# Optimization experiments

Measured on AMD Instinct MI355X. Metric: run time of the kernel, lower is better.

The kernel has to match this reference:

```python
import jax, jax.numpy as jnp
import numpy as np

N, NN, NI, ND, NH = 20000, 32, 128, 128, 8
RADIUS = 1.0
EPS = 1e-5


def _mlp(x, W1, b1, W2, b2):
    return jax.nn.elu(x @ W1 + b1) @ W2 + b2


def setup_inputs() -> dict:
    key = jax.random.key(0)
    ks = jax.random.split(key, 32)
    s = 0.05
    inp = {
        "features": jax.random.normal(ks[0], (N, NI), jnp.float32),
        "x": jax.random.normal(ks[1], (N, 3), jnp.float32),
        "nuv": jax.random.normal(ks[2], (N, 3, 3), jnp.float32),
        "topk": jax.random.randint(ks[3], (N, NN), 0, N, jnp.int64),
        # query_f: Ni -> Nd -> Nh*Nd
        "qW1": jax.random.normal(ks[4], (NI, ND), jnp.float32) * s,
        "qb1": jnp.zeros((ND,), jnp.float32),
        "qW2": jax.random.normal(ks[5], (ND, NH * ND), jnp.float32) * s,
        "qb2": jnp.zeros((NH * ND,), jnp.float32),
        # geo_encoder: 12 -> Nd -> Nd
        "gW1": jax.random.normal(ks[6], (12, ND), jnp.float32) * s,
        "gb1": jnp.zeros((ND,), jnp.float32),
        "gW2": jax.random.normal(ks[7], (ND, ND), jnp.float32) * s,
        "gb2": jnp.zeros((ND,), jnp.float32),
        # key_f / value_f: Nd -> Nd -> Nd
        "kW1": jax.random.normal(ks[8], (ND, ND), jnp.float32) * s,
        "kb1": jnp.zeros((ND,), jnp.float32),
        "kW2": jax.random.normal(ks[9], (ND, ND), jnp.float32) * s,
        "kb2": jnp.zeros((ND,), jnp.float32),
        "vW1": jax.random.normal(ks[10], (ND, ND), jnp.float32) * s,
        "vb1": jnp.zeros((ND,), jnp.float32),
        "vW2": jax.random.normal(ks[11], (ND, ND), jnp.float32) * s,
        "vb2": jnp.zeros((ND,), jnp.float32),
        # decode_f: Nh*Nd -> Nd -> Nd
        "dW1": jax.random.normal(ks[12], (NH * ND, ND), jnp.float32) * s,
        "db1": jnp.zeros((ND,), jnp.float32),
        "dW2": jax.random.normal(ks[13], (ND, ND), jnp.float32) * s,
        "db2": jnp.zeros((ND,), jnp.float32),
        # LayerNorm
        "ln_g": jnp.ones((ND,), jnp.float32),
        "ln_b": jnp.zeros((ND,), jnp.float32),
    }
    return inp


def reference(features, x, nuv, topk, qW1, qb1, qW2, qb2, gW1, gb1, gW2, gb2,
              kW1, kb1, kW2, kb2, vW1, vb1, vW2, vb2, dW1, db1, dW2, db2,
              ln_g, ln_b):
    n, nn = topk.shape
    sdk = jnp.sqrt(jnp.float32(ND))

    Q = _mlp(features, qW1, qb1, qW2, qb2).reshape(n, NH, ND)  # (N,Nh,Nd)

    features_nn = features[topk]              # (N,nn,Nd)
    x_nn = x[topk]                            # (N,nn,3)
    orient_x = x_nn - x[:, None, :]           # (N,nn,3)
    nuv_nn = nuv[topk].reshape(n, nn * 3, 3)  # (N,nn*3,3)

    dis2 = jnp.sum(orient_x * orient_x, axis=2, keepdims=True)
    dis = jnp.exp(-dis2 / (2.0 * RADIUS * RADIUS))  # (N,nn,1)

    # rotate neighbor offsets / frames into local frame: nuv @ v^T, then transpose
    RL_x = jnp.einsum('nij,nkj->nki', nuv, orient_x)            # (N,nn,3)
    RL_nuv = jnp.einsum('nij,nkj->nki', nuv, nuv_nn)            # (N,nn*3,3)
    RL_nuv = RL_nuv.reshape(n, nn, 9)
    RL = jnp.concatenate([RL_x, RL_nuv], axis=-1)               # (N,nn,12)

    geo_fea = _mlp(RL, gW1, gb1, gW2, gb2)
    geo_fea = dis * geo_fea * features_nn                       # (N,nn,Nd)

    K = _mlp(geo_fea, kW1, kb1, kW2, kb2)                       # (N,nn,Nd)
    V = _mlp(geo_fea, vW1, vb1, vW2, vb2)                       # (N,nn,Nd)

    Mq = jnp.einsum('nhd,nkd->nhk', Q, K)                       # (N,Nh,nn)
    mask = (topk == 0)[:, None, :]                              # (N,1,nn)
    Mq = jnp.where(mask, -jnp.inf, Mq)
    Mq = jax.nn.softmax(Mq / sdk, axis=2)

    out = jnp.einsum('nhk,nkd->nhd', Mq, V).reshape(n, NH * ND)
    out = _mlp(out, dW1, db1, dW2, db2) + features

    mu = jnp.mean(out, axis=-1, keepdims=True)
    var = jnp.var(out, axis=-1, keepdims=True)
    return (out - mu) / jnp.sqrt(var + EPS) * ln_g + ln_b
```

## Files before the change

kernel.cpp:

```cpp
#include <hip/hip_runtime.h>
#include <math.h>
#include <stdint.h>

#define ND 128
#define NNB 32
#define NH 8

typedef __attribute__((ext_vector_type(8))) short bf16x8;
typedef __attribute__((ext_vector_type(4))) float f32x4;
typedef __attribute__((ext_vector_type(8))) unsigned short u16x8;
typedef unsigned short u16;
typedef unsigned int u32;
typedef unsigned long long u64;

#define OFF_QW1T 0ULL
#define OFF_QW2T 32768ULL
#define OFF_GW1T 294912ULL
#define OFF_GW2T 303104ULL
#define OFF_KW1T 335872ULL
#define OFF_KW2T 368640ULL
#define OFF_VW1T 401408ULL
#define OFF_VW2T 434176ULL
#define OFF_DW1T 466944ULL
#define OFF_DW2T 729088ULL
#define OFF_Q    761856ULL
#define OFF_ATT  (OFF_Q + 20096ULL * 2048ULL)

__device__ __forceinline__ u16 rneb(float f){
    u32 u = __builtin_bit_cast(u32, f);
    u32 r = u + 0x7fffu + ((u >> 16) & 1u);
    return (u16)(r >> 16);
}
__device__ __forceinline__ float elu_f(float v){ return v > 0.f ? v : (__expf(v) - 1.f); }
__device__ __forceinline__ u64 pack4(float a, float b, float c, float d){
    return (u64)rneb(a) | ((u64)rneb(b) << 16) | ((u64)rneb(c) << 32) | ((u64)rneb(d) << 48);
}

#define GLDS16(g, l) __builtin_amdgcn_global_load_lds( \
    (const __attribute__((address_space(1))) u32*)(g), \
    (__attribute__((address_space(3))) u32*)(u32)(u64)(l), 16, 0, 0)

__device__ __forceinline__ void stage_rows(char* lds, const char* g, size_t gstride){
    const int t = threadIdx.x;
    const int seg = (t & 15) * 16, rr = t >> 4;
    #pragma unroll
    for (int i = 0; i < 8; i++){
        int row = i * 16 + rr;
        GLDS16(g + (size_t)row * gstride + seg, lds + row * 256 + seg);
    }
}

__device__ __forceinline__ bf16x8 ldfrag(const u16* base, int row, int kb, int l){
    int r = row + (l & 15);
    int byte = (r << 8) + (((kb << 1) + ((l >> 4) << 4)) ^ ((r & 7) << 4));
    return *(const bf16x8*)((const char*)base + byte);
}
__device__ __forceinline__ bf16x8 ldfragG(const char* __restrict__ Wt, int n, int kstride, int kb, int l){
    return *(const bf16x8*)(Wt + (size_t)(n + (l & 15)) * (size_t)kstride
                               + (size_t)((kb << 1) + ((l >> 4) << 4)));
}
__device__ __forceinline__ bf16x8 ldfragRL(const u16* base, int row, int l){
    int r = row + (l & 15);
    int byte = (r << 6) + ((((l >> 4) << 4)) ^ ((r & 3) << 4));
    return *(const bf16x8*)((const char*)base + byte);
}

__device__ __forceinline__ void store_cfrag(u16* out, int m0t, int n0t, int l, f32x4 v){
    int col = n0t + (l & 15);
    int r0 = m0t + ((l >> 4) << 2);
    #pragma unroll
    for (int j = 0; j < 4; j++){
        int r = r0 + j;
        int byte = (r << 8) + (((col << 1)) ^ ((r & 7) << 4));
        *(u16*)((char*)out + byte) = rneb(v[j]);
    }
}
__device__ __forceinline__ void store_cfragT(u16* out, int m0t, int n0t, int l, f32x4 v){
    int c = n0t + (l & 15);
    int r0 = m0t + ((l >> 4) << 2);
    *(u64*)((char*)out + (c << 8) + (((r0 << 1)) ^ ((c & 7) << 4))) = pack4(v[0], v[1], v[2], v[3]);
}

__device__ __forceinline__ void gemm_tileG(const u16* A, const char* __restrict__ Wt,
                                           int kstride, int kbase, f32x4 acc[4][4]){
    const int t = threadIdx.x, l = t & 63;
    const int m0 = ((t >> 7) & 1) * 64;
    const int n0 = ((t >> 6) & 1) * 64;
    bf16x8 b[4][4];
    #pragma unroll
    for (int kk = 0; kk < 4; kk++)
        #pragma unroll
        for (int i = 0; i < 4; i++)
            b[kk][i] = ldfragG(Wt, n0 + i * 16, kstride, kbase + kk * 32, l);
    #pragma unroll
    for (int kk = 0; kk < 4; kk++){
        bf16x8 a[4];
        #pragma unroll
        for (int i = 0; i < 4; i++) a[i] = ldfrag(A, m0 + i * 16, kk * 32, l);
        #pragma unroll
        for (int mt = 0; mt < 4; mt++)
            #pragma unroll
            for (int nt = 0; nt < 4; nt++)
                acc[mt][nt] = __builtin_amdgcn_mfma_f32_16x16x32_bf16(a[mt], b[kk][nt], acc[mt][nt], 0, 0, 0);
    }
}

struct PrepDesc {
    const float* src[10];
    u64 dstoff[10];
    int N[10], Ksrc[10], Kdst[10];
};

__global__ __launch_bounds__(256) void prep_weights(PrepDesc d, char* ws){
    int tid = blockIdx.x * 256 + threadIdx.x;
    #pragma unroll 1
    for (int m = 0; m < 10; m++){
        int cnt = (d.Kdst[m] * d.N[m]) >> 3;
        if (tid < cnt){
            int N = d.N[m];
            int nn = tid % N, k8 = tid / N;
            const float* s = d.src[m];
            u16x8 pk;
            #pragma unroll
            for (int i = 0; i < 8; i++){
                int k = k8 * 8 + i;
                pk[i] = (k < d.Ksrc[m]) ? rneb(s[(size_t)k * N + nn]) : (u16)0;
            }
            *(u16x8*)(ws + d.dstoff[m] + (u64)nn * (u64)(d.Kdst[m] * 2) + (u64)(k8 * 16)) = pk;
            return;
        }
        tid -= cnt;
    }
}

__global__ __launch_bounds__(256, 2) void qmlp_kernel(
    const float* __restrict__ F, const float* __restrict__ qb1, const float* __restrict__ qb2,
    const char* __restrict__ ws, u16* __restrict__ Qg, int n)
{
    __shared__ __align__(16) u16 sIn[16384];
    __shared__ __align__(16) u16 sH[16384];
    const int t = threadIdx.x;
    const int row0 = blockIdx.x * 128;
    const int l = t & 63;
    const int m0 = ((t >> 7) & 1) * 64;
    const int n0 = ((t >> 6) & 1) * 64;

    for (int i = t; i < 4096; i += 256){
        int r = i >> 5, c = (i & 31) * 4;
        int gr = row0 + r;
        float4 v = make_float4(0.f, 0.f, 0.f, 0.f);
        if (gr < n) v = *(const float4*)&F[(size_t)gr * ND + c];
        *(u64*)((char*)sIn + (r << 8) + (((c << 1)) ^ ((r & 7) << 4))) = pack4(v.x, v.y, v.z, v.w);
    }
    __syncthreads();

    f32x4 acc[4][4];
    #pragma unroll
    for (int i = 0; i < 4; i++)
        #pragma unroll
        for (int j = 0; j < 4; j++) acc[i][j] = 0.f;
    gemm_tileG(sIn, ws + OFF_QW1T, 256, 0, acc);
    #pragma unroll
    for (int mt = 0; mt < 4; mt++)
        #pragma unroll
        for (int nt = 0; nt < 4; nt++){
            int col = n0 + nt * 16 + (l & 15);
            float bv = qb1[col];
            f32x4 v;
            #pragma unroll
            for (int j = 0; j < 4; j++) v[j] = elu_f(acc[mt][nt][j] + bv);
            store_cfrag(sH, m0 + mt * 16, n0 + nt * 16, l, v);
        }
    __syncthreads();

    for (int ct = 0; ct < 8; ct++){
        f32x4 a2[4][4];
        #pragma unroll
        for (int i = 0; i < 4; i++)
            #pragma unroll
            for (int j = 0; j < 4; j++) a2[i][j] = 0.f;
        gemm_tileG(sH, ws + OFF_QW2T + (u64)ct * 32768ULL, 256, 0, a2);
        #pragma unroll
        for (int mt = 0; mt < 4; mt++)
            #pragma unroll
            for (int nt = 0; nt < 4; nt++){
                int col = n0 + nt * 16 + (l & 15);
                float bv = qb2[ct * 128 + col];
                int r0 = m0 + mt * 16 + ((l >> 4) << 2);
                #pragma unroll
                for (int j = 0; j < 4; j++)
                    *(u16*)((char*)sIn + ((r0 + j) << 8) + (col << 1)) = rneb(a2[mt][nt][j] + bv);
            }
        __syncthreads();
        {
            int row = t >> 1, half = t & 1;
            int gr = row0 + row;
            if (gr < n){
                const char* src = (const char*)sIn + (row << 8) + half * 128;
                char* dst = (char*)Qg + (size_t)gr * 2048 + ct * 256 + half * 128;
                #pragma unroll
                for (int i = 0; i < 8; i++)
                    *(uint4*)(dst + i * 16) = *(const uint4*)(src + i * 16);
            }
        }
        __syncthreads();
    }
}

template<int ACT>
__device__ __forceinline__ void layerG(
    const u16* inB, u16* outB, const char* __restrict__ Wt,
    const float* __restrict__ bias, const float* __restrict__ F,
    const int* sidx, const float* sdis)
{
    const int t = threadIdx.x, l = t & 63;
    const int m0 = ((t >> 7) & 1) * 64;
    const int n0 = ((t >> 6) & 1) * 64;
    f32x4 acc[4][4];
    #pragma unroll
    for (int i = 0; i < 4; i++)
        #pragma unroll
        for (int j = 0; j < 4; j++) acc[i][j] = 0.f;
    gemm_tileG(inB, Wt, 256, 0, acc);
    float fv[4][4][4];
    if (ACT == 2){
        #pragma unroll
        for (int mt = 0; mt < 4; mt++)
            #pragma unroll
            for (int nt = 0; nt < 4; nt++){
                int col = n0 + nt * 16 + (l & 15);
                int r0 = m0 + mt * 16 + ((l >> 4) << 2);
                #pragma unroll
                for (int j = 0; j < 4; j++){
                    int r = r0 + j;
                    fv[mt][nt][j] = sdis[r] * F[(size_t)sidx[r] * ND + col];
                }
            }
    }
    __syncthreads();
    #pragma unroll
    for (int mt = 0; mt < 4; mt++)
        #pragma unroll
        for (int nt = 0; nt < 4; nt++){
            int col = n0 + nt * 16 + (l & 15);
            float bv = bias[col];
            f32x4 v;
            #pragma unroll
            for (int j = 0; j < 4; j++){
                float x = acc[mt][nt][j] + bv;
                if (ACT == 1) x = elu_f(x);
                if (ACT == 2) x = x * fv[mt][nt][j];
                v[j] = x;
            }
            if (ACT == 3) store_cfragT(outB, m0 + mt * 16, n0 + nt * 16, l, v);
            else          store_cfrag (outB, m0 + mt * 16, n0 + nt * 16, l, v);
        }
    __syncthreads();
}

__global__ __launch_bounds__(256, 2) void attn_kernel(
    const float* __restrict__ F, const float* __restrict__ X,
    const float* __restrict__ NUV, const int* __restrict__ TOPK,
    const float* __restrict__ gb1, const float* __restrict__ gb2,
    const float* __restrict__ kb1, const float* __restrict__ kb2,
    const float* __restrict__ vb1, const float* __restrict__ vb2,
    const char* __restrict__ ws, const u16* __restrict__ Qg, u16* __restrict__ ATT)
{
    __shared__ __align__(16) u16 buf0[16384];
    __shared__ __align__(16) u16 buf1[16384];
    __shared__ __align__(16) u16 sP16[2560];
    __shared__ float sdis[128];
    __shared__ int   sidx[128];

    const int t = threadIdx.x;
    const int pid0 = blockIdx.x * 4;

    if (t < 128){
        int p = t >> 5, k = t & 31;
        int pid = pid0 + p;
        int idx = TOPK[(size_t)pid * NNB + k];
        sidx[t] = idx;
        float x0 = X[(size_t)pid * 3 + 0], x1 = X[(size_t)pid * 3 + 1], x2 = X[(size_t)pid * 3 + 2];
        float ox = X[(size_t)idx * 3 + 0] - x0;
        float oy = X[(size_t)idx * 3 + 1] - x1;
        float oz = X[(size_t)idx * 3 + 2] - x2;
        sdis[t] = __expf(-0.5f * (ox * ox + oy * oy + oz * oz));
        float nv[9];
        #pragma unroll
        for (int i = 0; i < 9; i++) nv[i] = NUV[(size_t)pid * 9 + i];
        float f[12];
        #pragma unroll
        for (int i = 0; i < 3; i++)
            f[i] = nv[i * 3 + 0] * ox + nv[i * 3 + 1] * oy + nv[i * 3 + 2] * oz;
        #pragma unroll
        for (int r = 0; r < 3; r++){
            float a0 = NUV[(size_t)idx * 9 + r * 3 + 0];
            float a1 = NUV[(size_t)idx * 9 + r * 3 + 1];
            float a2 = NUV[(size_t)idx * 9 + r * 3 + 2];
            #pragma unroll
            for (int i = 0; i < 3; i++)
                f[3 + r * 3 + i] = nv[i * 3 + 0] * a0 + nv[i * 3 + 1] * a1 + nv[i * 3 + 2] * a2;
        }
        char* rb = (char*)buf1 + (t << 6);
        u32 key = (u32)(t & 3) << 4;
        *(u64*)(rb + (0u ^ key))  = pack4(f[0], f[1], f[2], f[3]);
        *(u64*)(rb + (8u ^ key))  = pack4(f[4], f[5], f[6], f[7]);
        *(u64*)(rb + (16u ^ key)) = pack4(f[8], f[9], f[10], f[11]);
        *(u64*)(rb + (24u ^ key)) = 0ULL;
        *(u64*)(rb + (32u ^ key)) = 0ULL;
        *(u64*)(rb + (40u ^ key)) = 0ULL;
        *(u64*)(rb + (48u ^ key)) = 0ULL;
        *(u64*)(rb + (56u ^ key)) = 0ULL;
    }
    __syncthreads();

    {
        const int l = t & 63;
        const int m0 = ((t >> 7) & 1) * 64;
        const int n0 = ((t >> 6) & 1) * 64;
        bf16x8 bg[4], ag[4];
        #pragma unroll
        for (int i = 0; i < 4; i++) bg[i] = ldfragG(ws + OFF_GW1T, n0 + i * 16, 64, 0, l);
        #pragma unroll
        for (int i = 0; i < 4; i++) ag[i] = ldfragRL(buf1, m0 + i * 16, l);
        f32x4 acc[4][4];
        #pragma unroll
        for (int i = 0; i < 4; i++)
            #pragma unroll
            for (int j = 0; j < 4; j++) acc[i][j] = 0.f;
        #pragma unroll
        for (int mt = 0; mt < 4; mt++)
            #pragma unroll
            for (int nt = 0; nt < 4; nt++)
                acc[mt][nt] = __builtin_amdgcn_mfma_f32_16x16x32_bf16(ag[mt], bg[nt], acc[mt][nt], 0, 0, 0);
        #pragma unroll
        for (int mt = 0; mt < 4; mt++)
            #pragma unroll
            for (int nt = 0; nt < 4; nt++){
                int col = n0 + nt * 16 + (l & 15);
                float bv = gb1[col];
                f32x4 v;
                #pragma unroll
                for (int j = 0; j < 4; j++) v[j] = elu_f(acc[mt][nt][j] + bv);
                store_cfrag(buf0, m0 + mt * 16, n0 + nt * 16, l, v);
            }
    }
    __syncthreads();

    layerG<2>(buf0, buf0, ws + OFF_GW2T, gb2, F, sidx, sdis);
    layerG<1>(buf0, buf1, ws + OFF_KW1T, kb1, F, sidx, sdis);
    layerG<0>(buf1, buf1, ws + OFF_KW2T, kb2, F, sidx, sdis);
    layerG<1>(buf0, buf0, ws + OFF_VW1T, vb1, F, sidx, sdis);
    layerG<3>(buf0, buf0, ws + OFF_VW2T, vb2, F, sidx, sdis);

    {
        const int l = t & 63, w = t >> 6, hi = l >> 4;
        f32x4 s0, s1;
        s0 = 0.f; s1 = 0.f;
        const char* qb = (const char*)Qg + (size_t)(pid0 + w) * 2048
                       + (size_t)(l & 7) * 256 + (size_t)(hi << 4);
        #pragma unroll
        for (int kk = 0; kk < 4; kk++){
            bf16x8 bq = *(const bf16x8*)(qb + kk * 64);
            bf16x8 a0 = ldfrag(buf1, w * 32,      kk * 32, l);
            bf16x8 a1 = ldfrag(buf1, w * 32 + 16, kk * 32, l);
            s0 = __builtin_amdgcn_mfma_f32_16x16x32_bf16(a0, bq, s0, 0, 0, 0);
            s1 = __builtin_amdgcn_mfma_f32_16x16x32_bf16(a1, bq, s1, 0, 0, 0);
        }
        const float RS = 0.08838834764831845f;
        float sv[8];
        #pragma unroll
        for (int mt = 0; mt < 2; mt++)
            #pragma unroll
            for (int j = 0; j < 4; j++){
                int kidx = mt * 16 + (hi << 2) + j;
                float x = (mt ? s1[j] : s0[j]) * RS;
                if (sidx[w * 32 + kidx] == 0) x = -INFINITY;
                sv[mt * 4 + j] = x;
            }
        float mx = sv[0];
        #pragma unroll
        for (int i = 1; i < 8; i++) mx = fmaxf(mx, sv[i]);
        mx = fmaxf(mx, __shfl_xor(mx, 16));
        mx = fmaxf(mx, __shfl_xor(mx, 32));
        float e[8], sum = 0.f;
        #pragma unroll
        for (int i = 0; i < 8; i++){ e[i] = __expf(sv[i] - mx); sum += e[i]; }
        sum += __shfl_xor(sum, 16);
        sum += __shfl_xor(sum, 32);
        float inv = 1.f / sum;
        int h = l & 15;
        char* pb = (char*)sP16 + w * 1280 + h * 80 + hi * 8;
        *(u64*)(pb)      = pack4(e[0] * inv, e[1] * inv, e[2] * inv, e[3] * inv);
        *(u64*)(pb + 32) = pack4(e[4] * inv, e[5] * inv, e[6] * inv, e[7] * inv);
    }
    __syncthreads();

    {
        const int l = t & 63, w = t >> 6, hi = l >> 4;
        bf16x8 pa = *(const bf16x8*)((const char*)sP16 + w * 1280 + (l & 15) * 80 + (hi << 4));
        int pid = pid0 + w;
        u32 key = ((u32)pid & 7) << 4;
        char* dst = (char*)ATT + (size_t)pid * 2048;
        #pragma unroll
        for (int nt = 0; nt < 8; nt++){
            f32x4 o;
            o = 0.f;
            bf16x8 bv = ldfrag(buf0, nt * 16, w * 32, l);
            o = __builtin_amdgcn_mfma_f32_16x16x32_bf16(pa, bv, o, 0, 0, 0);
            if (hi < 2){
                int d = nt * 16 + (l & 15);
                #pragma unroll
                for (int j = 0; j < 4; j++){
                    int h = hi * 4 + j;
                    *(u16*)(dst + h * 256 + (((u32)(d << 1)) ^ key)) = rneb(o[j]);
                }
            }
        }
    }
}

__global__ __launch_bounds__(256, 2) void decode_kernel(
    const u16* __restrict__ ATT,
    const float* __restrict__ db1, const float* __restrict__ db2,
    const float* __restrict__ F,
    const float* __restrict__ lng, const float* __restrict__ lnb,
    const char* __restrict__ ws, float* __restrict__ OUT, int n)
{
    __shared__ __align__(16) char SM[67584];
    u16* sA = (u16*)SM;
    u16* sH = (u16*)(SM + 32768);
    float* sO = (float*)SM;

    const int t = threadIdx.x;
    const int row0 = blockIdx.x * 128;
    const int l = t & 63;
    const int m0 = ((t >> 7) & 1) * 64;
    const int n0 = ((t >> 6) & 1) * 64;

    f32x4 acc[4][4];
    #pragma unroll
    for (int i = 0; i < 4; i++)
        #pragma unroll
        for (int j = 0; j < 4; j++) acc[i][j] = 0.f;
    for (int kc = 0; kc < 8; kc++){
        stage_rows((char*)sA, (const char*)ATT + (size_t)row0 * 2048 + kc * 256, 2048);
        __syncthreads();
        gemm_tileG(sA, ws + OFF_DW1T, 2048, kc * 128, acc);
        __syncthreads();
    }
    #pragma unroll
    for (int mt = 0; mt < 4; mt++)
        #pragma unroll
        for (int nt = 0; nt < 4; nt++){
            int col = n0 + nt * 16 + (l & 15);
            float bv = db1[col];
            f32x4 v;
            #pragma unroll
            for (int j = 0; j < 4; j++) v[j] = elu_f(acc[mt][nt][j] + bv);
            store_cfrag(sH, m0 + mt * 16, n0 + nt * 16, l, v);
        }
    __syncthreads();

    f32x4 a2[4][4];
    #pragma unroll
    for (int i = 0; i < 4; i++)
        #pragma unroll
        for (int j = 0; j < 4; j++) a2[i][j] = 0.f;
    gemm_tileG(sH, ws + OFF_DW2T, 256, 0, a2);
    __syncthreads();

    #pragma unroll
    for (int mt = 0; mt < 4; mt++)
        #pragma unroll
        for (int nt = 0; nt < 4; nt++){
            int col = n0 + nt * 16 + (l & 15);
            float bv = db2[col];
            int r0 = m0 + mt * 16 + ((l >> 4) << 2);
            #pragma unroll
            for (int j = 0; j < 4; j++){
                int r = r0 + j;
                int gr = row0 + r;
                float x = a2[mt][nt][j] + bv;
                if (gr < n) x += F[(size_t)gr * ND + col];
                sO[r * 132 + col] = x;
            }
        }
    __syncthreads();

    {
        int r = t >> 1, half = t & 1;
        const float* rowp = sO + r * 132 + half * 64;
        float s = 0.f;
        #pragma unroll
        for (int i = 0; i < 16; i++){
            float4 v = ((const float4*)rowp)[i];
            s += v.x + v.y + v.z + v.w;
        }
        s += __shfl_xor(s, 1);
        float mu = s * (1.0f / 128.0f);
        float q = 0.f;
        #pragma unroll
        for (int i = 0; i < 16; i++){
            float4 v = ((const float4*)rowp)[i];
            q += (v.x - mu) * (v.x - mu) + (v.y - mu) * (v.y - mu)
               + (v.z - mu) * (v.z - mu) + (v.w - mu) * (v.w - mu);
        }
        q += __shfl_xor(q, 1);
        float rstd = rsqrtf(q * (1.0f / 128.0f) + 1e-5f);
        int gr = row0 + r;
        if (gr < n){
            #pragma unroll
            for (int i = 0; i < 16; i++){
                float4 v = ((const float4*)rowp)[i];
                int c = half * 64 + i * 4;
                float4 g4 = *(const float4*)&lng[c];
                float4 b4 = *(const float4*)&lnb[c];
                float4 ov = make_float4((v.x - mu) * rstd * g4.x + b4.x,
                                        (v.y - mu) * rstd * g4.y + b4.y,
                                        (v.z - mu) * rstd * g4.z + b4.z,
                                        (v.w - mu) * rstd * g4.w + b4.w);
                *(float4*)&OUT[(size_t)gr * ND + c] = ov;
            }
        }
    }
}

extern "C" void kernel_launch(void* const* d_in, const int* in_sizes, int n_in,
                              void* d_out, int out_size, void* d_ws, size_t ws_size,
                              hipStream_t stream)
{
    const float* F    = (const float*)d_in[0];
    const float* X    = (const float*)d_in[1];
    const float* NUV  = (const float*)d_in[2];
    const int*   TOPK = (const int*)d_in[3];
    const float* qW1  = (const float*)d_in[4];
    const float* qb1  = (const float*)d_in[5];
    const float* qW2  = (const float*)d_in[6];
    const float* qb2  = (const float*)d_in[7];
    const float* gW1  = (const float*)d_in[8];
    const float* gb1  = (const float*)d_in[9];
    const float* gW2  = (const float*)d_in[10];
    const float* gb2  = (const float*)d_in[11];
    const float* kW1  = (const float*)d_in[12];
    const float* kb1  = (const float*)d_in[13];
    const float* kW2  = (const float*)d_in[14];
    const float* kb2  = (const float*)d_in[15];
    const float* vW1  = (const float*)d_in[16];
    const float* vb1  = (const float*)d_in[17];
    const float* vW2  = (const float*)d_in[18];
    const float* vb2  = (const float*)d_in[19];
    const float* dW1  = (const float*)d_in[20];
    const float* db1  = (const float*)d_in[21];
    const float* dW2  = (const float*)d_in[22];
    const float* db2  = (const float*)d_in[23];
    const float* lng  = (const float*)d_in[24];
    const float* lnb  = (const float*)d_in[25];

    const int n = in_sizes[0] / ND;
    char* wsb = (char*)d_ws;

    PrepDesc pd;
    const float* srcs[10] = {qW1, qW2, gW1, gW2, kW1, kW2, vW1, vW2, dW1, dW2};
    u64 offs[10] = {OFF_QW1T, OFF_QW2T, OFF_GW1T, OFF_GW2T, OFF_KW1T,
                    OFF_KW2T, OFF_VW1T, OFF_VW2T, OFF_DW1T, OFF_DW2T};
    int Ns[10]   = {128, 1024, 128, 128, 128, 128, 128, 128, 128, 128};
    int Ksrc[10] = {128, 128, 12, 128, 128, 128, 128, 128, 1024, 128};
    int Kdst[10] = {128, 128, 32, 128, 128, 128, 128, 128, 1024, 128};
    for (int i = 0; i < 10; i++){
        pd.src[i] = srcs[i]; pd.dstoff[i] = offs[i];
        pd.N[i] = Ns[i]; pd.Ksrc[i] = Ksrc[i]; pd.Kdst[i] = Kdst[i];
    }
    prep_weights<<<186, 256, 0, stream>>>(pd, wsb);

    u16* Qg  = (u16*)(wsb + OFF_Q);
    u16* ATT = (u16*)(wsb + OFF_ATT);
    const int nb = (n + 127) / 128;

    qmlp_kernel<<<nb, 256, 0, stream>>>(F, qb1, qb2, wsb, Qg, n);
    attn_kernel<<<n / 4, 256, 0, stream>>>(F, X, NUV, TOPK, gb1, gb2,
                                           kb1, kb2, vb1, vb2, wsb, Qg, ATT);
    decode_kernel<<<nb, 256, 0, stream>>>(ATT, db1, db2, F, lng, lnb, wsb, (float*)d_out, n);
}
```

Measured before the change: 410.5 us.

## Swap GEMM operand roles so epilogues write packed transposed outputs

Adds a gemm_WA form in which the weight fragment is the MFMA A operand and the activation is B. Each lane then holds four consecutive output channels of one row, so bias loads become float4, stores become packed 64-bit writes, and gathers of F become vector loads. The attention kernel is reordered: the V MLP now runs after the softmax, using a separate buffer instead of in-place passes, which removes some barriers. s_setprio is wrapped around the MFMA loops. This adds layout complexity and risks LDS bank conflicts on the new store pattern.

```diff
diff --git a/kernel.cpp b/kernel.cpp
--- a/kernel.cpp
+++ b/kernel.cpp
@@ -65,33 +65,44 @@
     return *(const bf16x8*)((const char*)base + byte);
 }
 
-__device__ __forceinline__ void store_cfrag(u16* out, int m0t, int n0t, int l, f32x4 v){
-    int col = n0t + (l & 15);
-    int r0 = m0t + ((l >> 4) << 2);
-    #pragma unroll
-    for (int j = 0; j < 4; j++){
-        int r = r0 + j;
-        int byte = (r << 8) + (((col << 1)) ^ ((r & 7) << 4));
-        *(u16*)((char*)out + byte) = rneb(v[j]);
-    }
-}
-__device__ __forceinline__ void store_cfragT(u16* out, int m0t, int n0t, int l, f32x4 v){
-    int c = n0t + (l & 15);
-    int r0 = m0t + ((l >> 4) << 2);
-    *(u64*)((char*)out + (c << 8) + (((r0 << 1)) ^ ((c & 7) << 4))) = pack4(v[0], v[1], v[2], v[3]);
-}
-
-__device__ __forceinline__ void gemm_tileG(const u16* A, const char* __restrict__ Wt,
-                                           int kstride, int kbase, f32x4 acc[4][4]){
+__device__ __forceinline__ void gemm_WA(const char* __restrict__ Wt, int kstride, int kbase,
+                                        const u16* B, f32x4 acc[4][4]){
     const int t = threadIdx.x, l = t & 63;
     const int m0 = ((t >> 7) & 1) * 64;
     const int n0 = ((t >> 6) & 1) * 64;
-    bf16x8 b[4][4];
+    bf16x8 aw[4][4];
     #pragma unroll
     for (int kk = 0; kk < 4; kk++)
         #pragma unroll
         for (int i = 0; i < 4; i++)
-            b[kk][i] = ldfragG(Wt, n0 + i * 16, kstride, kbase + kk * 32, l);
+            aw[kk][i] = ldfragG(Wt, m0 + i * 16, kstride, kbase + kk * 32, l);
+    __builtin_amdgcn_s_setprio(1);
+    #pragma unroll
+    for (int kk = 0; kk < 4; kk++){
+        bf16x8 b[4];
+        #pragma unroll
+        for (int i = 0; i < 4; i++) b[i] = ldfrag(B, n0 + i * 16, kk * 32, l);
+        #pragma unroll
+        for (int mt = 0; mt < 4; mt++)
+            #pragma unroll
+            for (int nt = 0; nt < 4; nt++)
+                acc[mt][nt] = __builtin_amdgcn_mfma_f32_16x16x32_bf16(aw[kk][mt], b[nt], acc[mt][nt], 0, 0, 0);
+    }
+    __builtin_amdgcn_s_setprio(0);
+}
+
+__device__ __forceinline__ void gemm_AW(const u16* A, const char* __restrict__ Wt,
+                                        f32x4 acc[4][4]){
+    const int t = threadIdx.x, l = t & 63;
+    const int m0 = ((t >> 7) & 1) * 64;
+    const int n0 = ((t >> 6) & 1) * 64;
+    bf16x8 bw[4][4];
+    #pragma unroll
+    for (int kk = 0; kk < 4; kk++)
+        #pragma unroll
+        for (int i = 0; i < 4; i++)
+            bw[kk][i] = ldfragG(Wt, n0 + i * 16, 256, kk * 32, l);
+    __builtin_amdgcn_s_setprio(1);
     #pragma unroll
     for (int kk = 0; kk < 4; kk++){
         bf16x8 a[4];
@@ -101,8 +112,9 @@
         for (int mt = 0; mt < 4; mt++)
             #pragma unroll
             for (int nt = 0; nt < 4; nt++)
-                acc[mt][nt] = __builtin_amdgcn_mfma_f32_16x16x32_bf16(a[mt], b[kk][nt], acc[mt][nt], 0, 0, 0);
-    }
+                acc[mt][nt] = __builtin_amdgcn_mfma_f32_16x16x32_bf16(a[mt], bw[kk][nt], acc[mt][nt], 0, 0, 0);
+    }
+    __builtin_amdgcn_s_setprio(0);
 }
 
 struct PrepDesc {
@@ -144,6 +156,7 @@
     const int l = t & 63;
     const int m0 = ((t >> 7) & 1) * 64;
     const int n0 = ((t >> 6) & 1) * 64;
+    const int hi = l >> 4;
 
     for (int i = t; i < 4096; i += 256){
         int r = i >> 5, c = (i & 31) * 4;
@@ -159,18 +172,19 @@
     for (int i = 0; i < 4; i++)
         #pragma unroll
         for (int j = 0; j < 4; j++) acc[i][j] = 0.f;
-    gemm_tileG(sIn, ws + OFF_QW1T, 256, 0, acc);
-    #pragma unroll
-    for (int mt = 0; mt < 4; mt++)
+    gemm_WA(ws + OFF_QW1T, 256, 0, sIn, acc);
+    #pragma unroll
+    for (int mt = 0; mt < 4; mt++){
+        int ch0 = m0 + mt * 16 + (hi << 2);
+        float4 bq = *(const float4*)&qb1[ch0];
         #pragma unroll
         for (int nt = 0; nt < 4; nt++){
-            int col = n0 + nt * 16 + (l & 15);
-            float bv = qb1[col];
-            f32x4 v;
-            #pragma unroll
-            for (int j = 0; j < 4; j++) v[j] = elu_f(acc[mt][nt][j] + bv);
-            store_cfrag(sH, m0 + mt * 16, n0 + nt * 16, l, v);
-        }
+            int xrow = n0 + nt * 16 + (l & 15);
+            u64 pk = pack4(elu_f(acc[mt][nt][0] + bq.x), elu_f(acc[mt][nt][1] + bq.y),
+                           elu_f(acc[mt][nt][2] + bq.z), elu_f(acc[mt][nt][3] + bq.w));
+            *(u64*)((char*)sH + (xrow << 8) + (((ch0 << 1)) ^ ((xrow & 7) << 4))) = pk;
+        }
+    }
     __syncthreads();
 
     for (int ct = 0; ct < 8; ct++){
@@ -179,18 +193,19 @@
         for (int i = 0; i < 4; i++)
             #pragma unroll
             for (int j = 0; j < 4; j++) a2[i][j] = 0.f;
-        gemm_tileG(sH, ws + OFF_QW2T + (u64)ct * 32768ULL, 256, 0, a2);
-        #pragma unroll
-        for (int mt = 0; mt < 4; mt++)
+        gemm_WA(ws + OFF_QW2T + (u64)ct * 32768ULL, 256, 0, sH, a2);
+        #pragma unroll
+        for (int mt = 0; mt < 4; mt++){
+            int ch0 = m0 + mt * 16 + (hi << 2);
+            float4 bq = *(const float4*)&qb2[ct * 128 + ch0];
             #pragma unroll
             for (int nt = 0; nt < 4; nt++){
-                int col = n0 + nt * 16 + (l & 15);
-                float bv = qb2[ct * 128 + col];
-                int r0 = m0 + mt * 16 + ((l >> 4) << 2);
-                #pragma unroll
-                for (int j = 0; j < 4; j++)
-                    *(u16*)((char*)sIn + ((r0 + j) << 8) + (col << 1)) = rneb(a2[mt][nt][j] + bv);
-            }
+                int xrow = n0 + nt * 16 + (l & 15);
+                *(u64*)((char*)sIn + (xrow << 8) + (ch0 << 1)) =
+                    pack4(a2[mt][nt][0] + bq.x, a2[mt][nt][1] + bq.y,
+                          a2[mt][nt][2] + bq.z, a2[mt][nt][3] + bq.w);
+            }
+        }
         __syncthreads();
         {
             int row = t >> 1, half = t & 1;
@@ -207,8 +222,8 @@
     }
 }
 
-template<int ACT>
-__device__ __forceinline__ void layerG(
+template<int ACT, bool INPLACE>
+__device__ __forceinline__ void layerW(
     const u16* inB, u16* outB, const char* __restrict__ Wt,
     const float* __restrict__ bias, const float* __restrict__ F,
     const int* sidx, const float* sdis)
@@ -216,45 +231,38 @@
     const int t = threadIdx.x, l = t & 63;
     const int m0 = ((t >> 7) & 1) * 64;
     const int n0 = ((t >> 6) & 1) * 64;
+    const int hi = l >> 4;
     f32x4 acc[4][4];
     #pragma unroll
     for (int i = 0; i < 4; i++)
         #pragma unroll
         for (int j = 0; j < 4; j++) acc[i][j] = 0.f;
-    gemm_tileG(inB, Wt, 256, 0, acc);
-    float fv[4][4][4];
-    if (ACT == 2){
-        #pragma unroll
-        for (int mt = 0; mt < 4; mt++)
-            #pragma unroll
-            for (int nt = 0; nt < 4; nt++){
-                int col = n0 + nt * 16 + (l & 15);
-                int r0 = m0 + mt * 16 + ((l >> 4) << 2);
+    gemm_WA(Wt, 256, 0, inB, acc);
+    if (INPLACE) __syncthreads();
+    #pragma unroll
+    for (int mt = 0; mt < 4; mt++){
+        int ch0 = m0 + mt * 16 + (hi << 2);
+        float4 bq = *(const float4*)&bias[ch0];
+        #pragma unroll
+        for (int nt = 0; nt < 4; nt++){
+            int xrow = n0 + nt * 16 + (l & 15);
+            float v[4];
+            #pragma unroll
+            for (int j = 0; j < 4; j++) v[j] = acc[mt][nt][j] + ((const float*)&bq)[j];
+            if (ACT == 1){
                 #pragma unroll
-                for (int j = 0; j < 4; j++){
-                    int r = r0 + j;
-                    fv[mt][nt][j] = sdis[r] * F[(size_t)sidx[r] * ND + col];
-                }
-            }
-    }
-    __syncthreads();
-    #pragma unroll
-    for (int mt = 0; mt < 4; mt++)
-        #pragma unroll
-        for (int nt = 0; nt < 4; nt++){
-            int col = n0 + nt * 16 + (l & 15);
-            float bv = bias[col];
-            f32x4 v;
-            #pragma unroll
-            for (int j = 0; j < 4; j++){
-                float x = acc[mt][nt][j] + bv;
-                if (ACT == 1) x = elu_f(x);
-                if (ACT == 2) x = x * fv[mt][nt][j];
-                v[j] = x;
-            }
-            if (ACT == 3) store_cfragT(outB, m0 + mt * 16, n0 + nt * 16, l, v);
-            else          store_cfrag (outB, m0 + mt * 16, n0 + nt * 16, l, v);
-        }
+                for (int j = 0; j < 4; j++) v[j] = elu_f(v[j]);
+            }
+            if (ACT == 2){
+                float dsc = sdis[xrow];
+                float4 fq = *(const float4*)&F[(size_t)sidx[xrow] * ND + ch0];
+                #pragma unroll
+                for (int j = 0; j < 4; j++) v[j] *= dsc * ((const float*)&fq)[j];
+            }
+            *(u64*)((char*)outB + (xrow << 8) + (((ch0 << 1)) ^ ((xrow & 7) << 4))) =
+                pack4(v[0], v[1], v[2], v[3]);
+        }
+    }
     __syncthreads();
 }
 
@@ -266,14 +274,16 @@
     const float* __restrict__ vb1, const float* __restrict__ vb2,
     const char* __restrict__ ws, const u16* __restrict__ Qg, u16* __restrict__ ATT)
 {
-    __shared__ __align__(16) u16 buf0[16384];
-    __shared__ __align__(16) u16 buf1[16384];
-    __shared__ __align__(16) u16 sP16[2560];
+    __shared__ __align__(16) u16 bufA[16384];
+    __shared__ __align__(16) u16 bufB[16384];
+    __shared__ __align__(16) u16 sP16[2048];
     __shared__ float sdis[128];
     __shared__ int   sidx[128];
 
     const int t = threadIdx.x;
     const int pid0 = blockIdx.x * 4;
+    const int l = t & 63;
+    const int hi = l >> 4;
 
     if (t < 128){
         int p = t >> 5, k = t & 31;
@@ -301,7 +311,7 @@
             for (int i = 0; i < 3; i++)
                 f[3 + r * 3 + i] = nv[i * 3 + 0] * a0 + nv[i * 3 + 1] * a1 + nv[i * 3 + 2] * a2;
         }
-        char* rb = (char*)buf1 + (t << 6);
+        char* rb = (char*)bufB + (t << 6);
         u32 key = (u32)(t & 3) << 4;
         *(u64*)(rb + (0u ^ key))  = pack4(f[0], f[1], f[2], f[3]);
         *(u64*)(rb + (8u ^ key))  = pack4(f[4], f[5], f[6], f[7]);
@@ -315,46 +325,46 @@
     __syncthreads();
 
     {
-        const int l = t & 63;
         const int m0 = ((t >> 7) & 1) * 64;
         const int n0 = ((t >> 6) & 1) * 64;
-        bf16x8 bg[4], ag[4];
-        #pragma unroll
-        for (int i = 0; i < 4; i++) bg[i] = ldfragG(ws + OFF_GW1T, n0 + i * 16, 64, 0, l);
-        #pragma unroll
-        for (int i = 0; i < 4; i++) ag[i] = ldfragRL(buf1, m0 + i * 16, l);
+        bf16x8 ag[4], bg[4];
+        #pragma unroll
+        for (int i = 0; i < 4; i++) ag[i] = ldfragG(ws + OFF_GW1T, m0 + i * 16, 64, 0, l);
+        #pragma unroll
+        for (int i = 0; i < 4; i++) bg[i] = ldfragRL(bufB, n0 + i * 16, l);
         f32x4 acc[4][4];
         #pragma unroll
         for (int i = 0; i < 4; i++)
             #pragma unroll
             for (int j = 0; j < 4; j++) acc[i][j] = 0.f;
+        __builtin_amdgcn_s_setprio(1);
         #pragma unroll
         for (int mt = 0; mt < 4; mt++)
             #pragma unroll
             for (int nt = 0; nt < 4; nt++)
                 acc[mt][nt] = __builtin_amdgcn_mfma_f32_16x16x32_bf16(ag[mt], bg[nt], acc[mt][nt], 0, 0, 0);
-        #pragma unroll
-        for (int mt = 0; mt < 4; mt++)
+        __builtin_amdgcn_s_setprio(0);
+        #pragma unroll
+        for (int mt = 0; mt < 4; mt++){
+            int ch0 = m0 + mt * 16 + (hi << 2);
+            float4 bq = *(const float4*)&gb1[ch0];
             #pragma unroll
             for (int nt = 0; nt < 4; nt++){
-                int col = n0 + nt * 16 + (l & 15);
-                float bv = gb1[col];
-                f32x4 v;
-                #pragma unroll
-                for (int j = 0; j < 4; j++) v[j] = elu_f(acc[mt][nt][j] + bv);
-                store_cfrag(buf0, m0 + mt * 16, n0 + nt * 16, l, v);
-            }
-    }
-    __syncthreads();
-
-    layerG<2>(buf0, buf0, ws + OFF_GW2T, gb2, F, sidx, sdis);
-    layerG<1>(buf0, buf1, ws + OFF_KW1T, kb1, F, sidx, sdis);
-    layerG<0>(buf1, buf1, ws + OFF_KW2T, kb2, F, sidx, sdis);
-    layerG<1>(buf0, buf0, ws + OFF_VW1T, vb1, F, sidx, sdis);
-    layerG<3>(buf0, buf0, ws + OFF_VW2T, vb2, F, sidx, sdis);
+                int xrow = n0 + nt * 16 + (l & 15);
+                u64 pk = pack4(elu_f(acc[mt][nt][0] + bq.x), elu_f(acc[mt][nt][1] + bq.y),
+                               elu_f(acc[mt][nt][2] + bq.z), elu_f(acc[mt][nt][3] + bq.w));
+                *(u64*)((char*)bufA + (xrow << 8) + (((ch0 << 1)) ^ ((xrow & 7) << 4))) = pk;
+            }
+        }
+    }
+    __syncthreads();
+
+    layerW<2, false>(bufA, bufB, ws + OFF_GW2T, gb2, F, sidx, sdis);
+    layerW<1, false>(bufB, bufA, ws + OFF_KW1T, kb1, F, sidx, sdis);
+    layerW<0, true >(bufA, bufA, ws + OFF_KW2T, kb2, F, sidx, sdis);
 
     {
-        const int l = t & 63, w = t >> 6, hi = l >> 4;
+        const int w = t >> 6;
         f32x4 s0, s1;
         s0 = 0.f; s1 = 0.f;
         const char* qb = (const char*)Qg + (size_t)(pid0 + w) * 2048
@@ -362,8 +372,8 @@
         #pragma unroll
         for (int kk = 0; kk < 4; kk++){
             bf16x8 bq = *(const bf16x8*)(qb + kk * 64);
-            bf16x8 a0 = ldfrag(buf1, w * 32,      kk * 32, l);
-            bf16x8 a1 = ldfrag(buf1, w * 32 + 16, kk * 32, l);
+            bf16x8 a0 = ldfrag(bufA, w * 32,      kk * 32, l);
+            bf16x8 a1 = ldfrag(bufA, w * 32 + 16, kk * 32, l);
             s0 = __builtin_amdgcn_mfma_f32_16x16x32_bf16(a0, bq, s0, 0, 0, 0);
             s1 = __builtin_amdgcn_mfma_f32_16x16x32_bf16(a1, bq, s1, 0, 0, 0);
         }
@@ -389,32 +399,53 @@
         sum += __shfl_xor(sum, 16);
         sum += __shfl_xor(sum, 32);
         float inv = 1.f / sum;
-        int h = l & 15;
-        char* pb = (char*)sP16 + w * 1280 + h * 80 + hi * 8;
+        char* pb = (char*)sP16 + w * 1024 + (l & 15) * 64 + hi * 8;
         *(u64*)(pb)      = pack4(e[0] * inv, e[1] * inv, e[2] * inv, e[3] * inv);
         *(u64*)(pb + 32) = pack4(e[4] * inv, e[5] * inv, e[6] * inv, e[7] * inv);
     }
     __syncthreads();
 
+    layerW<1, false>(bufB, bufA, ws + OFF_VW1T, vb1, F, sidx, sdis);
+
     {
-        const int l = t & 63, w = t >> 6, hi = l >> 4;
-        bf16x8 pa = *(const bf16x8*)((const char*)sP16 + w * 1280 + (l & 15) * 80 + (hi << 4));
+        const int m0 = ((t >> 7) & 1) * 64;
+        const int n0 = ((t >> 6) & 1) * 64;
+        f32x4 a2[4][4];
+        #pragma unroll
+        for (int i = 0; i < 4; i++)
+            #pragma unroll
+            for (int j = 0; j < 4; j++) a2[i][j] = 0.f;
+        gemm_AW(bufA, ws + OFF_VW2T, a2);
+        #pragma unroll
+        for (int mt = 0; mt < 4; mt++)
+            #pragma unroll
+            for (int nt = 0; nt < 4; nt++){
+                int ch = n0 + nt * 16 + (l & 15);
+                float bv = vb2[ch];
+                int r0 = m0 + mt * 16 + (hi << 2);
+                *(u64*)((char*)bufB + (ch << 8) + (((r0 << 1)) ^ ((ch & 7) << 4))) =
+                    pack4(a2[mt][nt][0] + bv, a2[mt][nt][1] + bv,
+                          a2[mt][nt][2] + bv, a2[mt][nt][3] + bv);
+            }
+    }
+    __syncthreads();
+
+    {
+        const int w = t >> 6;
         int pid = pid0 + w;
         u32 key = ((u32)pid & 7) << 4;
         char* dst = (char*)ATT + (size_t)pid * 2048;
+        const bf16x8 pb = *(const bf16x8*)((const char*)sP16 + w * 1024 + (l & 15) * 64 + (hi << 4));
+        int h = l & 15;
         #pragma unroll
         for (int nt = 0; nt < 8; nt++){
             f32x4 o;
             o = 0.f;
-            bf16x8 bv = ldfrag(buf0, nt * 16, w * 32, l);
-            o = __builtin_amdgcn_mfma_f32_16x16x32_bf16(pa, bv, o, 0, 0, 0);
-            if (hi < 2){
-                int d = nt * 16 + (l & 15);
-                #pragma unroll
-                for (int j = 0; j < 4; j++){
-                    int h = hi * 4 + j;
-                    *(u16*)(dst + h * 256 + (((u32)(d << 1)) ^ key)) = rneb(o[j]);
-                }
+            bf16x8 av = ldfrag(bufB, nt * 16, w * 32, l);
+            o = __builtin_amdgcn_mfma_f32_16x16x32_bf16(av, pb, o, 0, 0, 0);
+            if (h < 8){
+                u32 dbyte = (u32)(nt * 32 + hi * 8);
+                *(u64*)(dst + h * 256 + (dbyte ^ key)) = pack4(o[0], o[1], o[2], o[3]);
             }
         }
     }
@@ -437,6 +468,7 @@
     const int l = t & 63;
     const int m0 = ((t >> 7) & 1) * 64;
     const int n0 = ((t >> 6) & 1) * 64;
+    const int hi = l >> 4;
 
     f32x4 acc[4][4];
     #pragma unroll
@@ -446,20 +478,21 @@
     for (int kc = 0; kc < 8; kc++){
         stage_rows((char*)sA, (const char*)ATT + (size_t)row0 * 2048 + kc * 256, 2048);
         __syncthreads();
-        gemm_tileG(sA, ws + OFF_DW1T, 2048, kc * 128, acc);
+        gemm_WA(ws + OFF_DW1T, 2048, kc * 128, sA, acc);
         __syncthreads();
     }
     #pragma unroll
-    for (int mt = 0; mt < 4; mt++)
+    for (int mt = 0; mt < 4; mt++){
+        int ch0 = m0 + mt * 16 + (hi << 2);
+        float4 bq = *(const float4*)&db1[ch0];
         #pragma unroll
         for (int nt = 0; nt < 4; nt++){
-            int col = n0 + nt * 16 + (l & 15);
-            float bv = db1[col];
-            f32x4 v;
-            #pragma unroll
-            for (int j = 0; j < 4; j++) v[j] = elu_f(acc[mt][nt][j] + bv);
-            store_cfrag(sH, m0 + mt * 16, n0 + nt * 16, l, v);
-        }
+            int xrow = n0 + nt * 16 + (l & 15);
+            u64 pk = pack4(elu_f(acc[mt][nt][0] + bq.x), elu_f(acc[mt][nt][1] + bq.y),
+                           elu_f(acc[mt][nt][2] + bq.z), elu_f(acc[mt][nt][3] + bq.w));
+            *(u64*)((char*)sH + (xrow << 8) + (((ch0 << 1)) ^ ((xrow & 7) << 4))) = pk;
+        }
+    }
     __syncthreads();
 
     f32x4 a2[4][4];
@@ -467,25 +500,26 @@
     for (int i = 0; i < 4; i++)
         #pragma unroll
         for (int j = 0; j < 4; j++) a2[i][j] = 0.f;
-    gemm_tileG(sH, ws + OFF_DW2T, 256, 0, a2);
-    __syncthreads();
-
-    #pragma unroll
-    for (int mt = 0; mt < 4; mt++)
+    gemm_WA(ws + OFF_DW2T, 256, 0, sH, a2);
+    __syncthreads();
+
+    #pragma unroll
+    for (int mt = 0; mt < 4; mt++){
+        int ch0 = m0 + mt * 16 + (hi << 2);
+        float4 bq = *(const float4*)&db2[ch0];
         #pragma unroll
         for (int nt = 0; nt < 4; nt++){
-            int col = n0 + nt * 16 + (l & 15);
-            float bv = db2[col];
-            int r0 = m0 + mt * 16 + ((l >> 4) << 2);
-            #pragma unroll
-            for (int j = 0; j < 4; j++){
-                int r = r0 + j;
-                int gr = row0 + r;
-                float x = a2[mt][nt][j] + bv;
-                if (gr < n) x += F[(size_t)gr * ND + col];
-                sO[r * 132 + col] = x;
-            }
-        }
+            int xrow = n0 + nt * 16 + (l & 15);
+            int gr = row0 + xrow;
+            float4 fres = make_float4(0.f, 0.f, 0.f, 0.f);
+            if (gr < n) fres = *(const float4*)&F[(size_t)gr * ND + ch0];
+            float4 ov = make_float4(a2[mt][nt][0] + bq.x + fres.x,
+                                    a2[mt][nt][1] + bq.y + fres.y,
+                                    a2[mt][nt][2] + bq.z + fres.z,
+                                    a2[mt][nt][3] + bq.w + fres.w);
+            *(float4*)&sO[xrow * 132 + ch0] = ov;
+        }
+    }
     __syncthreads();
 
     {
```

Result: slower. 422.7 us (+3.0%).
